# Kernel optimization log

Measured on AMD Instinct MI355X. Metric: run time of the kernel, lower is better.

The kernel has to match this reference:

```python
import jax, jax.numpy as jnp
import numpy as np

NUM_HEADS = 16
HEAD_DIM = 64
LN_EPS = 1e-5


def setup_inputs() -> dict:
    key = jax.random.key(0)
    k1, k2, k3, k4 = jax.random.split(key, 4)
    B, N, D = 4, 2048, NUM_HEADS * HEAD_DIM
    q = jax.random.normal(k1, (B, N, D), dtype=jnp.float32)
    k = jax.random.normal(k2, (B, N, D), dtype=jnp.float32)
    v = jax.random.normal(k3, (B, N, D), dtype=jnp.float32)
    W_out = jax.random.normal(k4, (D, D), dtype=jnp.float32) * (1.0 / np.sqrt(D))
    g = jnp.ones((D,), dtype=jnp.float32)
    return {"q": q, "k": k, "v": v, "W_out": W_out, "g": g}


def _split_heads(x):
    b, n, _ = x.shape
    return x.reshape(b, n, NUM_HEADS, HEAD_DIM).transpose(0, 2, 1, 3)  # b h n d


def reference(q, k, v, W_out, g):
    scale = HEAD_DIM ** -0.5
    qh = _split_heads(q) * scale          # [b,h,n,d]
    kh = _split_heads(k)                  # [b,h,m,d]
    vh = _split_heads(v)                  # [b,h,m,d]
    sim = jnp.einsum('bhnd,bhmd->bhnm', qh, kh)
    attn = jax.nn.softmax(sim.astype(jnp.float32), axis=-1)
    out = jnp.einsum('bhnm,bhmd->bhnd', attn, vh)
    b, h, n, d = out.shape
    out = out.transpose(0, 2, 1, 3).reshape(b, n, h * d)  # b n (h d)
    out = out @ W_out.T                   # Linear, no bias
    # LayerNorm (bias=False), biased variance
    mean = jnp.mean(out, axis=-1, keepdims=True)
    var = jnp.var(out, axis=-1, keepdims=True)
    return (out - mean) * jax.lax.rsqrt(var + LN_EPS) * g
```

## Files before the change

kernel.cpp:

```cpp
#include <hip/hip_runtime.h>
#include <hip/hip_bf16.h>


#define Bv 4
#define Nv 2048
#define Hv 16
#define DHv 64
#define Dv 1024
#define NT (Nv / 64)

typedef __attribute__((ext_vector_type(8))) short short8;
typedef __attribute__((ext_vector_type(4))) float floatx4;

__device__ inline unsigned pack_bf2(float a, float b) {
    unsigned ua = __builtin_bit_cast(unsigned, a) + 0x8000u;
    unsigned ub = __builtin_bit_cast(unsigned, b) + 0x8000u;
    return __builtin_amdgcn_perm(ub, ua, 0x07060302u);
}

__global__ __launch_bounds__(256)
void attn_mfma(const float* __restrict__ q,
               const float* __restrict__ k,
               const float* __restrict__ v,
               __hip_bfloat16* __restrict__ out) {
    __shared__ __align__(16) short Kt[2][64 * 64];
    __shared__ __align__(16) short Vt[2][64 * 64];

    const int t = threadIdx.x;
    const int wave = t >> 6, lane = t & 63;
    const int quad = lane >> 4, lr = lane & 15;
    const int b = blockIdx.z, h = blockIdx.y;
    const int q0 = blockIdx.x * 128;
    const size_t bh = ((size_t)b * Nv) * Dv + h * DHv;

    float4 kpre[2][2], vpre[2][2];
    auto load_tile = [&](int k0) {
#pragma unroll
        for (int p = 0; p < 2; ++p) {
            int idx = p * 256 + t;
            int r = idx >> 3, cb = idx & 7;
            const float* kp = k + bh + (size_t)(k0 + r) * Dv + cb * 8;
            kpre[p][0] = *(const float4*)kp;
            kpre[p][1] = *(const float4*)(kp + 4);
            int dq = idx & 15, rr = idx >> 4;
            const float* vp = v + bh + (size_t)(k0 + 2 * rr) * Dv + dq * 4;
            vpre[p][0] = *(const float4*)vp;
            vpre[p][1] = *(const float4*)(vp + Dv);
        }
    };
    auto store_tile = [&](int buf) {
#pragma unroll
        for (int p = 0; p < 2; ++p) {
            int idx = p * 256 + t;
            int r = idx >> 3, cb = idx & 7;
            uint4 u;
            u.x = pack_bf2(kpre[p][0].x, kpre[p][0].y);
            u.y = pack_bf2(kpre[p][0].z, kpre[p][0].w);
            u.z = pack_bf2(kpre[p][1].x, kpre[p][1].y);
            u.w = pack_bf2(kpre[p][1].z, kpre[p][1].w);
            *(uint4*)&Kt[buf][r * 64 + ((cb ^ (r & 7)) << 3)] = u;
            int dq = idx & 15, rr = idx >> 4;
            float va[4] = {vpre[p][0].x, vpre[p][0].y, vpre[p][0].z, vpre[p][0].w};
            float vb[4] = {vpre[p][1].x, vpre[p][1].y, vpre[p][1].z, vpre[p][1].w};
#pragma unroll
            for (int i = 0; i < 4; ++i) {
                int d = dq * 4 + i;
                ((unsigned*)Vt[buf])[d * 32 + (((rr >> 2) ^ ((d >> 1) & 7)) << 2) + (rr & 3)] =
                    pack_bf2(va[i], vb[i]);
            }
        }
    };

    load_tile(0);

    short8 qfrag[2][2];
#pragma unroll
    for (int qs = 0; qs < 2; ++qs)
#pragma unroll
        for (int kh = 0; kh < 2; ++kh) {
            int row = q0 + wave * 32 + qs * 16 + lr;
            const float* qp = q + bh + (size_t)row * Dv + kh * 32 + quad * 8;
            float4 f0 = *(const float4*)qp;
            float4 f1 = *(const float4*)(qp + 4);
            int4 qi;
            qi.x = (int)pack_bf2(f0.x * 0.125f, f0.y * 0.125f);
            qi.y = (int)pack_bf2(f0.z * 0.125f, f0.w * 0.125f);
            qi.z = (int)pack_bf2(f1.x * 0.125f, f1.y * 0.125f);
            qi.w = (int)pack_bf2(f1.z * 0.125f, f1.w * 0.125f);
            qfrag[qs][kh] = __builtin_bit_cast(short8, qi);
        }

    store_tile(0);

    floatx4 o_acc[2][4] = {};
    float mrow[2] = {-INFINITY, -INFINITY};
    float lrow[2] = {0.f, 0.f};
    const int srcA = ((2 * (quad & 1)) << 4) | lr;
    const int srcB = srcA + 16;
    const bool hi = (quad >= 2);

    for (int it = 0; it < NT; ++it) {
        const int cur = it & 1;
        __syncthreads();
        if (it + 1 < NT) load_tile((it + 1) * 64);

        floatx4 s_acc[2][4] = {};
#pragma unroll
        for (int tt = 0; tt < 4; ++tt) {
            int row = tt * 16 + lr;
            short8 kf0 = *(const short8*)&Kt[cur][row * 64 + ((quad ^ (lr & 7)) << 3)];
            short8 kf1 = *(const short8*)&Kt[cur][row * 64 + (((4 + quad) ^ (lr & 7)) << 3)];
#pragma unroll
            for (int qs = 0; qs < 2; ++qs) {
                s_acc[qs][tt] = __builtin_amdgcn_mfma_f32_16x16x32_bf16(kf0, qfrag[qs][0], s_acc[qs][tt], 0, 0, 0);
                s_acc[qs][tt] = __builtin_amdgcn_mfma_f32_16x16x32_bf16(kf1, qfrag[qs][1], s_acc[qs][tt], 0, 0, 0);
            }
        }

        unsigned p2[2][8];
#pragma unroll
        for (int qs = 0; qs < 2; ++qs) {
            float tmax = -INFINITY;
#pragma unroll
            for (int tt = 0; tt < 4; ++tt)
#pragma unroll
                for (int r2 = 0; r2 < 4; ++r2) tmax = fmaxf(tmax, s_acc[qs][tt][r2]);
            tmax = fmaxf(tmax, __shfl_xor(tmax, 16));
            tmax = fmaxf(tmax, __shfl_xor(tmax, 32));
            float mnew = fmaxf(mrow[qs], tmax);
            float alpha = __expf(mrow[qs] - mnew);
            mrow[qs] = mnew;
            float psum = 0.f;
#pragma unroll
            for (int tt = 0; tt < 4; ++tt)
#pragma unroll
                for (int r2 = 0; r2 < 4; ++r2) {
                    float p = __expf(s_acc[qs][tt][r2] - mnew);
                    s_acc[qs][tt][r2] = p;
                    psum += p;
                }
            psum += __shfl_xor(psum, 16);
            psum += __shfl_xor(psum, 32);
            lrow[qs] = lrow[qs] * alpha + psum;
#pragma unroll
            for (int r2 = 0; r2 < 4; ++r2) {
                float ar = __shfl(alpha, quad * 4 + r2);
#pragma unroll
                for (int td = 0; td < 4; ++td) o_acc[qs][td][r2] *= ar;
            }
#pragma unroll
            for (int tt = 0; tt < 4; ++tt) {
                p2[qs][tt * 2 + 0] = pack_bf2(s_acc[qs][tt][0], s_acc[qs][tt][1]);
                p2[qs][tt * 2 + 1] = pack_bf2(s_acc[qs][tt][2], s_acc[qs][tt][3]);
            }
        }

#pragma unroll
        for (int kh = 0; kh < 2; ++kh) {
            short8 af[2];
#pragma unroll
            for (int qs = 0; qs < 2; ++qs) {
                int tlo = 4 * kh, thi = 4 * kh + 2;
                unsigned d0a = __shfl(p2[qs][tlo + 0], srcA), d0b = __shfl(p2[qs][thi + 0], srcA);
                unsigned d1a = __shfl(p2[qs][tlo + 1], srcA), d1b = __shfl(p2[qs][thi + 1], srcA);
                unsigned d2a = __shfl(p2[qs][tlo + 0], srcB), d2b = __shfl(p2[qs][thi + 0], srcB);
                unsigned d3a = __shfl(p2[qs][tlo + 1], srcB), d3b = __shfl(p2[qs][thi + 1], srcB);
                int4 afi;
                afi.x = (int)(hi ? d0b : d0a);
                afi.y = (int)(hi ? d1b : d1a);
                afi.z = (int)(hi ? d2b : d2a);
                afi.w = (int)(hi ? d3b : d3a);
                af[qs] = __builtin_bit_cast(short8, afi);
            }
#pragma unroll
            for (int td = 0; td < 4; ++td) {
                int d = td * 16 + lr;
                short8 vf = *(const short8*)&Vt[cur][d * 64 + (((kh * 4 + quad) ^ (lr >> 1)) << 3)];
                o_acc[0][td] = __builtin_amdgcn_mfma_f32_16x16x32_bf16(af[0], vf, o_acc[0][td], 0, 0, 0);
                o_acc[1][td] = __builtin_amdgcn_mfma_f32_16x16x32_bf16(af[1], vf, o_acc[1][td], 0, 0, 0);
            }
        }

        if (it + 1 < NT) store_tile(1 - cur);
    }

#pragma unroll
    for (int qs = 0; qs < 2; ++qs) {
        float linv = 1.f / lrow[qs];
#pragma unroll
        for (int r2 = 0; r2 < 4; ++r2) {
            float lv = __shfl(linv, quad * 4 + r2);
            int row = q0 + wave * 32 + qs * 16 + quad * 4 + r2;
            size_t base = ((size_t)(b * Nv + row)) * Dv + h * DHv;
#pragma unroll
            for (int td = 0; td < 4; ++td)
                out[base + td * 16 + lr] = __float2bfloat16(o_acc[qs][td][r2] * lv);
        }
    }
}

__global__ __launch_bounds__(256)
void proj_kernel(const __hip_bfloat16* __restrict__ A,
                 const float* __restrict__ W,
                 float* __restrict__ C) {
    __shared__ __align__(16) short As[2][128 * 32];
    __shared__ __align__(16) short Ws[2][128 * 32];

    const int t = threadIdx.x;
    const int wave = t >> 6, lane = t & 63;
    const int quad = lane >> 4, lr = lane & 15;
    const int wm = wave >> 1, wn = wave & 1;
    const int bm = blockIdx.y * 128;
    const int bn = blockIdx.x * 128;

    floatx4 acc[4][4] = {};

    const int rA = t >> 2;
    const int cbA = t & 3;

    uint4 apre[2];
    float4 wpre[2][2];
    auto load_t = [&](int k0) {
#pragma unroll
        for (int p = 0; p < 2; ++p) {
            int r = rA + p * 64;
            apre[p] = *(const uint4*)(A + (size_t)(bm + r) * Dv + k0 + cbA * 8);
            const float* wp = W + (size_t)(bn + r) * Dv + k0 + cbA * 8;
            wpre[p][0] = *(const float4*)wp;
            wpre[p][1] = *(const float4*)(wp + 4);
        }
    };
    auto store_t = [&](int buf) {
#pragma unroll
        for (int p = 0; p < 2; ++p) {
            int r = rA + p * 64;
            *(uint4*)&As[buf][r * 32 + cbA * 8] = apre[p];
            uint4 u;
            u.x = pack_bf2(wpre[p][0].x, wpre[p][0].y);
            u.y = pack_bf2(wpre[p][0].z, wpre[p][0].w);
            u.z = pack_bf2(wpre[p][1].x, wpre[p][1].y);
            u.w = pack_bf2(wpre[p][1].z, wpre[p][1].w);
            *(uint4*)&Ws[buf][r * 32 + cbA * 8] = u;
        }
    };

    load_t(0);
    store_t(0);

    for (int it = 0; it < Dv / 32; ++it) {
        const int cur = it & 1;
        __syncthreads();
        if (it + 1 < Dv / 32) load_t((it + 1) * 32);

        short8 af[4];
#pragma unroll
        for (int mb = 0; mb < 4; ++mb)
            af[mb] = *(const short8*)&As[cur][(wm * 64 + mb * 16 + lr) * 32 + quad * 8];
#pragma unroll
        for (int nb = 0; nb < 4; ++nb) {
            short8 bf = *(const short8*)&Ws[cur][(wn * 64 + nb * 16 + lr) * 32 + quad * 8];
#pragma unroll
            for (int mb = 0; mb < 4; ++mb)
                acc[mb][nb] = __builtin_amdgcn_mfma_f32_16x16x32_bf16(af[mb], bf, acc[mb][nb], 0, 0, 0);
        }

        if (it + 1 < Dv / 32) store_t(1 - cur);
    }

#pragma unroll
    for (int mb = 0; mb < 4; ++mb)
#pragma unroll
        for (int nb = 0; nb < 4; ++nb) {
            int row = bm + wm * 64 + mb * 16 + quad * 4;
            int col = bn + wn * 64 + nb * 16 + lr;
#pragma unroll
            for (int r = 0; r < 4; ++r)
                C[(size_t)(row + r) * Dv + col] = acc[mb][nb][r];
        }
}

__global__ __launch_bounds__(256)
void ln_kernel(float* __restrict__ C,
               const float* __restrict__ g) {
    const int row = blockIdx.x;
    const int t = threadIdx.x;
    const int wave = t >> 6, lane = t & 63;

    float* rp = C + (size_t)row * Dv;
    float4 x = *(const float4*)(rp + t * 4);

    float s = x.x + x.y + x.z + x.w;
    float sq = x.x * x.x + x.y * x.y + x.z * x.z + x.w * x.w;
#pragma unroll
    for (int off = 32; off >= 1; off >>= 1) {
        s += __shfl_xor(s, off);
        sq += __shfl_xor(sq, off);
    }
    __shared__ float ss[4], ssq[4];
    if (lane == 0) { ss[wave] = s; ssq[wave] = sq; }
    __syncthreads();
    s = ss[0] + ss[1] + ss[2] + ss[3];
    sq = ssq[0] + ssq[1] + ssq[2] + ssq[3];

    const float rn = 1.f / (float)Dv;
    float mean = s * rn;
    float var = sq * rn - mean * mean;
    float inv = rsqrtf(var + 1e-5f);

    float4 gv = *(const float4*)(g + t * 4);

    float4 o;
    o.x = (x.x - mean) * inv * gv.x;
    o.y = (x.y - mean) * inv * gv.y;
    o.z = (x.z - mean) * inv * gv.z;
    o.w = (x.w - mean) * inv * gv.w;
    *(float4*)(rp + t * 4) = o;
}

extern "C" void kernel_launch(void* const* d_in, const int* in_sizes, int n_in,
                              void* d_out, int out_size, void* d_ws, size_t ws_size,
                              hipStream_t stream) {
    const float* q = (const float*)d_in[0];
    const float* k = (const float*)d_in[1];
    const float* v = (const float*)d_in[2];
    const float* W = (const float*)d_in[3];
    const float* g = (const float*)d_in[4];
    float* out = (float*)d_out;

    __hip_bfloat16* attn = (__hip_bfloat16*)d_ws;

    attn_mfma<<<dim3(Nv / 128, Hv, Bv), 256, 0, stream>>>(q, k, v, attn);
    proj_kernel<<<dim3(Dv / 128, (Bv * Nv) / 128), 256, 0, stream>>>(attn, W, out);
    ln_kernel<<<Bv * Nv, 256, 0, stream>>>(out, g);
}
```

Before: 337.5 us.

## Pre-convert W to bf16 and stream projection tiles via direct global-to-LDS loads

Adds a small kernel that converts W_out to bf16 once per call into workspace. A new projection GEMM uses global_load_lds to move A and W tiles straight into XOR-swizzled LDS with a K-tile of 64 and double buffering. This removes the per-tile fp32-to-bf16 conversion and register staging in the GEMM, and halves W traffic. The cost is an extra kernel launch and workspace use. The old fp32-W path is kept as a fallback when the workspace is too small.

```diff
diff --git a/kernel.cpp b/kernel.cpp
--- a/kernel.cpp
+++ b/kernel.cpp
@@ -200,9 +200,95 @@
 }
 
 __global__ __launch_bounds__(256)
+void wconv_kernel(const float* __restrict__ W, __hip_bfloat16* __restrict__ Wb) {
+    int base = (blockIdx.x * 256 + threadIdx.x) * 8;
+    float4 f0 = *(const float4*)(W + base);
+    float4 f1 = *(const float4*)(W + base + 4);
+    uint4 u;
+    u.x = pack_bf2(f0.x, f0.y);
+    u.y = pack_bf2(f0.z, f0.w);
+    u.z = pack_bf2(f1.x, f1.y);
+    u.w = pack_bf2(f1.z, f1.w);
+    *(uint4*)(Wb + base) = u;
+}
+
+__global__ __launch_bounds__(256)
 void proj_kernel(const __hip_bfloat16* __restrict__ A,
-                 const float* __restrict__ W,
+                 const __hip_bfloat16* __restrict__ Wb,
                  float* __restrict__ C) {
+    __shared__ __align__(16) short As[2][128 * 64];
+    __shared__ __align__(16) short Ws[2][128 * 64];
+
+    const int t = threadIdx.x;
+    const int wave = t >> 6, lane = t & 63;
+    const int quad = lane >> 4, lr = lane & 15;
+    const int wm = wave >> 1, wn = wave & 1;
+    const int bm = blockIdx.y * 128;
+    const int bn = blockIdx.x * 128;
+
+    floatx4 acc[4][4] = {};
+
+    auto stage = [&](int buf, int k0) {
+#pragma unroll
+        for (int c = 0; c < 4; ++c) {
+            const int blk = c * 4 + wave;
+            const int r = blk * 8 + (lane >> 3);
+            const int g = (lane & 7) ^ (r & 7);
+            const __hip_bfloat16* ga = A + (size_t)(bm + r) * Dv + k0 + g * 8;
+            const __hip_bfloat16* gw = Wb + (size_t)(bn + r) * Dv + k0 + g * 8;
+            __builtin_amdgcn_global_load_lds(
+                (const __attribute__((address_space(1))) unsigned int*)(const void*)ga,
+                (__attribute__((address_space(3))) unsigned int*)(void*)&As[buf][blk * 512],
+                16, 0, 0);
+            __builtin_amdgcn_global_load_lds(
+                (const __attribute__((address_space(1))) unsigned int*)(const void*)gw,
+                (__attribute__((address_space(3))) unsigned int*)(void*)&Ws[buf][blk * 512],
+                16, 0, 0);
+        }
+    };
+
+    stage(0, 0);
+
+    for (int it = 0; it < Dv / 64; ++it) {
+        const int cur = it & 1;
+        __syncthreads();
+        if (it + 1 < Dv / 64) stage(1 - cur, (it + 1) * 64);
+
+#pragma unroll
+        for (int ks = 0; ks < 2; ++ks) {
+            short8 af[4];
+#pragma unroll
+            for (int mb = 0; mb < 4; ++mb) {
+                int row = wm * 64 + mb * 16 + lr;
+                af[mb] = *(const short8*)&As[cur][row * 64 + (((ks * 4 + quad) ^ (lr & 7)) << 3)];
+            }
+#pragma unroll
+            for (int nb = 0; nb < 4; ++nb) {
+                int row = wn * 64 + nb * 16 + lr;
+                short8 bf = *(const short8*)&Ws[cur][row * 64 + (((ks * 4 + quad) ^ (lr & 7)) << 3)];
+#pragma unroll
+                for (int mb = 0; mb < 4; ++mb)
+                    acc[mb][nb] = __builtin_amdgcn_mfma_f32_16x16x32_bf16(af[mb], bf, acc[mb][nb], 0, 0, 0);
+            }
+        }
+    }
+
+#pragma unroll
+    for (int mb = 0; mb < 4; ++mb)
+#pragma unroll
+        for (int nb = 0; nb < 4; ++nb) {
+            int row = bm + wm * 64 + mb * 16 + quad * 4;
+            int col = bn + wn * 64 + nb * 16 + lr;
+#pragma unroll
+            for (int r = 0; r < 4; ++r)
+                C[(size_t)(row + r) * Dv + col] = acc[mb][nb][r];
+        }
+}
+
+__global__ __launch_bounds__(256)
+void proj_kernel_f32w(const __hip_bfloat16* __restrict__ A,
+                      const float* __restrict__ W,
+                      float* __restrict__ C) {
     __shared__ __align__(16) short As[2][128 * 32];
     __shared__ __align__(16) short Ws[2][128 * 32];
 
@@ -327,9 +413,20 @@
     const float* g = (const float*)d_in[4];
     float* out = (float*)d_out;
 
+    const size_t attnBytes = (size_t)Bv * Nv * Dv * 2;
+    const size_t wbBytes = (size_t)Dv * Dv * 2;
+
     __hip_bfloat16* attn = (__hip_bfloat16*)d_ws;
 
     attn_mfma<<<dim3(Nv / 128, Hv, Bv), 256, 0, stream>>>(q, k, v, attn);
-    proj_kernel<<<dim3(Dv / 128, (Bv * Nv) / 128), 256, 0, stream>>>(attn, W, out);
+
+    if (ws_size >= attnBytes + wbBytes) {
+        __hip_bfloat16* Wb = (__hip_bfloat16*)((char*)d_ws + attnBytes);
+        wconv_kernel<<<512, 256, 0, stream>>>(W, Wb);
+        proj_kernel<<<dim3(Dv / 128, (Bv * Nv) / 128), 256, 0, stream>>>(attn, Wb, out);
+    } else {
+        proj_kernel_f32w<<<dim3(Dv / 128, (Bv * Nv) / 128), 256, 0, stream>>>(attn, W, out);
+    }
+
     ln_kernel<<<Bv * Nv, 256, 0, stream>>>(out, g);
 }
```

Result: faster. 318.8 us (-5.5%).

## Pre-convert K, V, W to bf16 and stage tiles via direct global-to-LDS loads

Applied to the files above, without the earlier changes.

Adds a prep kernel that converts K and W to bf16 and writes V transposed per head in bf16. The attention and projection kernels then fill LDS with global_load_lds DMA into swizzled layouts, with no register round-trip or per-tile conversion. The projection K-step grows to 64, attention blocks are remapped so heads group by XCD, and shuffle-based reductions and P-fragment exchanges use permlane swaps. This costs an extra kernel launch and an extra read and write of K, V and W through workspace memory.

```diff
diff --git a/kernel.cpp b/kernel.cpp
--- a/kernel.cpp
+++ b/kernel.cpp
@@ -9,6 +9,10 @@
 #define Dv 1024
 #define NT (Nv / 64)
 
+#define KCONV_BLOCKS 4096
+#define WCONV_BLOCKS 512
+#define VT_BLOCKS 2048
+
 typedef __attribute__((ext_vector_type(8))) short short8;
 typedef __attribute__((ext_vector_type(4))) float floatx4;
 
@@ -18,60 +22,125 @@
     return __builtin_amdgcn_perm(ub, ua, 0x07060302u);
 }
 
+__device__ inline void plswap16(unsigned &a, unsigned &b) {
+    auto r = __builtin_amdgcn_permlane16_swap(a, b, false, false);
+    a = r[0]; b = r[1];
+}
+__device__ inline void plswap32(unsigned &a, unsigned &b) {
+    auto r = __builtin_amdgcn_permlane32_swap(a, b, false, false);
+    a = r[0]; b = r[1];
+}
+
+__device__ inline float redq_max(float x) {
+    unsigned a = __builtin_bit_cast(unsigned, x), b = a;
+    plswap16(a, b);
+    float m = fmaxf(__builtin_bit_cast(float, a), __builtin_bit_cast(float, b));
+    unsigned c = __builtin_bit_cast(unsigned, m), d = c;
+    plswap32(c, d);
+    return fmaxf(__builtin_bit_cast(float, c), __builtin_bit_cast(float, d));
+}
+__device__ inline float redq_sum(float x) {
+    unsigned a = __builtin_bit_cast(unsigned, x), b = a;
+    plswap16(a, b);
+    float m = __builtin_bit_cast(float, a) + __builtin_bit_cast(float, b);
+    unsigned c = __builtin_bit_cast(unsigned, m), d = c;
+    plswap32(c, d);
+    return __builtin_bit_cast(float, c) + __builtin_bit_cast(float, d);
+}
+
 __global__ __launch_bounds__(256)
-void attn_mfma(const float* __restrict__ q,
-               const float* __restrict__ k,
-               const float* __restrict__ v,
-               __hip_bfloat16* __restrict__ out) {
+void prep_all(const float* __restrict__ K, __hip_bfloat16* __restrict__ Kb,
+              const float* __restrict__ W, __hip_bfloat16* __restrict__ Wb,
+              const float* __restrict__ v, __hip_bfloat16* __restrict__ vt) {
+    __shared__ short T[64][72];
+    int bid = blockIdx.x;
+    if (bid < KCONV_BLOCKS + WCONV_BLOCKS) {
+        const float* src;
+        __hip_bfloat16* dst;
+        if (bid < KCONV_BLOCKS) { src = K; dst = Kb; }
+        else { src = W; dst = Wb; bid -= KCONV_BLOCKS; }
+        int base = (bid * 256 + threadIdx.x) * 8;
+        float4 f0 = *(const float4*)(src + base);
+        float4 f1 = *(const float4*)(src + base + 4);
+        uint4 u;
+        u.x = pack_bf2(f0.x, f0.y);
+        u.y = pack_bf2(f0.z, f0.w);
+        u.z = pack_bf2(f1.x, f1.y);
+        u.w = pack_bf2(f1.z, f1.w);
+        *(uint4*)(dst + base) = u;
+        return;
+    }
+    bid -= KCONV_BLOCKS + WCONV_BLOCKS;
+    const int b = bid >> 9;
+    const int rem = bid & 511;
+    const int h = rem >> 5;
+    const int n0 = (rem & 31) * 64;
+    const int t = threadIdx.x;
+    const int ir = t >> 4;
+    const int d4 = (t & 15) * 4;
+#pragma unroll
+    for (int pass = 0; pass < 4; ++pass) {
+        int n = pass * 16 + ir;
+        float4 f = *(const float4*)(v + ((size_t)b * Nv + n0 + n) * Dv + h * DHv + d4);
+        T[d4 + 0][n] = (short)(pack_bf2(f.x, f.x) & 0xffffu);
+        T[d4 + 1][n] = (short)(pack_bf2(f.y, f.y) & 0xffffu);
+        T[d4 + 2][n] = (short)(pack_bf2(f.z, f.z) & 0xffffu);
+        T[d4 + 3][n] = (short)(pack_bf2(f.w, f.w) & 0xffffu);
+    }
+    __syncthreads();
+    const int d = t >> 2, kg = (t & 3) * 16;
+    unsigned u[8];
+#pragma unroll
+    for (int i = 0; i < 8; ++i)
+        u[i] = (unsigned)(unsigned short)T[d][kg + 2 * i] |
+               ((unsigned)(unsigned short)T[d][kg + 2 * i + 1] << 16);
+    __hip_bfloat16* op = vt + ((size_t)(b * Hv + h) * DHv + d) * Nv + n0 + kg;
+    *(uint4*)op = *(uint4*)&u[0];
+    *(uint4*)(op + 8) = *(uint4*)&u[4];
+}
+
+__global__ __launch_bounds__(256)
+void attn_mfma_pre(const float* __restrict__ q,
+                   const __hip_bfloat16* __restrict__ Kb,
+                   const __hip_bfloat16* __restrict__ Vtb,
+                   __hip_bfloat16* __restrict__ out) {
     __shared__ __align__(16) short Kt[2][64 * 64];
     __shared__ __align__(16) short Vt[2][64 * 64];
 
     const int t = threadIdx.x;
     const int wave = t >> 6, lane = t & 63;
     const int quad = lane >> 4, lr = lane & 15;
-    const int b = blockIdx.z, h = blockIdx.y;
-    const int q0 = blockIdx.x * 128;
-    const size_t bh = ((size_t)b * Nv) * Dv + h * DHv;
-
-    float4 kpre[2][2], vpre[2][2];
-    auto load_tile = [&](int k0) {
-#pragma unroll
-        for (int p = 0; p < 2; ++p) {
-            int idx = p * 256 + t;
-            int r = idx >> 3, cb = idx & 7;
-            const float* kp = k + bh + (size_t)(k0 + r) * Dv + cb * 8;
-            kpre[p][0] = *(const float4*)kp;
-            kpre[p][1] = *(const float4*)(kp + 4);
-            int dq = idx & 15, rr = idx >> 4;
-            const float* vp = v + bh + (size_t)(k0 + 2 * rr) * Dv + dq * 4;
-            vpre[p][0] = *(const float4*)vp;
-            vpre[p][1] = *(const float4*)(vp + Dv);
+    const int b = blockIdx.z;
+    const int lid2 = blockIdx.y * 16 + blockIdx.x;
+    const int xcd = lid2 & 7, jj = lid2 >> 3;
+    const int h = xcd * 2 + (jj >> 4);
+    const int q0 = (jj & 15) * 128;
+    const size_t qbh = ((size_t)b * Nv) * Dv + h * DHv;
+    const __hip_bfloat16* kb = Kb + (size_t)b * Nv * Dv + h * DHv;
+    const __hip_bfloat16* vtb = Vtb + (size_t)(b * Hv + h) * DHv * Nv;
+
+    const int srow = lane >> 3;
+    const int sg = lane & 7;
+    auto stage = [&](int buf, int k0) {
+#pragma unroll
+        for (int c = 0; c < 2; ++c) {
+            int blk = wave * 2 + c;
+            int r = blk * 8 + srow;
+            int g = sg ^ (r & 7);
+            __builtin_amdgcn_global_load_lds(
+                (const __attribute__((address_space(1))) unsigned*)(const void*)
+                    (kb + (size_t)(k0 + r) * Dv + g * 8),
+                (__attribute__((address_space(3))) unsigned*)(void*)&Kt[buf][blk * 512],
+                16, 0, 0);
+            __builtin_amdgcn_global_load_lds(
+                (const __attribute__((address_space(1))) unsigned*)(const void*)
+                    (vtb + (size_t)r * Nv + k0 + g * 8),
+                (__attribute__((address_space(3))) unsigned*)(void*)&Vt[buf][blk * 512],
+                16, 0, 0);
         }
     };
-    auto store_tile = [&](int buf) {
-#pragma unroll
-        for (int p = 0; p < 2; ++p) {
-            int idx = p * 256 + t;
-            int r = idx >> 3, cb = idx & 7;
-            uint4 u;
-            u.x = pack_bf2(kpre[p][0].x, kpre[p][0].y);
-            u.y = pack_bf2(kpre[p][0].z, kpre[p][0].w);
-            u.z = pack_bf2(kpre[p][1].x, kpre[p][1].y);
-            u.w = pack_bf2(kpre[p][1].z, kpre[p][1].w);
-            *(uint4*)&Kt[buf][r * 64 + ((cb ^ (r & 7)) << 3)] = u;
-            int dq = idx & 15, rr = idx >> 4;
-            float va[4] = {vpre[p][0].x, vpre[p][0].y, vpre[p][0].z, vpre[p][0].w};
-            float vb[4] = {vpre[p][1].x, vpre[p][1].y, vpre[p][1].z, vpre[p][1].w};
-#pragma unroll
-            for (int i = 0; i < 4; ++i) {
-                int d = dq * 4 + i;
-                ((unsigned*)Vt[buf])[d * 32 + (((rr >> 2) ^ ((d >> 1) & 7)) << 2) + (rr & 3)] =
-                    pack_bf2(va[i], vb[i]);
-            }
-        }
-    };
-
-    load_tile(0);
+
+    stage(0, 0);
 
     short8 qfrag[2][2];
 #pragma unroll
@@ -79,7 +148,7 @@
 #pragma unroll
         for (int kh = 0; kh < 2; ++kh) {
             int row = q0 + wave * 32 + qs * 16 + lr;
-            const float* qp = q + bh + (size_t)row * Dv + kh * 32 + quad * 8;
+            const float* qp = q + qbh + (size_t)row * Dv + kh * 32 + quad * 8;
             float4 f0 = *(const float4*)qp;
             float4 f1 = *(const float4*)(qp + 4);
             int4 qi;
@@ -90,19 +159,14 @@
             qfrag[qs][kh] = __builtin_bit_cast(short8, qi);
         }
 
-    store_tile(0);
-
     floatx4 o_acc[2][4] = {};
     float mrow[2] = {-INFINITY, -INFINITY};
     float lrow[2] = {0.f, 0.f};
-    const int srcA = ((2 * (quad & 1)) << 4) | lr;
-    const int srcB = srcA + 16;
-    const bool hi = (quad >= 2);
 
     for (int it = 0; it < NT; ++it) {
         const int cur = it & 1;
         __syncthreads();
-        if (it + 1 < NT) load_tile((it + 1) * 64);
+        if (it + 1 < NT) stage(1 - cur, (it + 1) * 64);
 
         floatx4 s_acc[2][4] = {};
 #pragma unroll
@@ -120,13 +184,13 @@
         unsigned p2[2][8];
 #pragma unroll
         for (int qs = 0; qs < 2; ++qs) {
-            float tmax = -INFINITY;
+            float t4[4];
 #pragma unroll
             for (int tt = 0; tt < 4; ++tt)
-#pragma unroll
-                for (int r2 = 0; r2 < 4; ++r2) tmax = fmaxf(tmax, s_acc[qs][tt][r2]);
-            tmax = fmaxf(tmax, __shfl_xor(tmax, 16));
-            tmax = fmaxf(tmax, __shfl_xor(tmax, 32));
+                t4[tt] = fmaxf(fmaxf(s_acc[qs][tt][0], s_acc[qs][tt][1]),
+                               fmaxf(s_acc[qs][tt][2], s_acc[qs][tt][3]));
+            float tmax = fmaxf(fmaxf(t4[0], t4[1]), fmaxf(t4[2], t4[3]));
+            tmax = redq_max(tmax);
             float mnew = fmaxf(mrow[qs], tmax);
             float alpha = __expf(mrow[qs] - mnew);
             mrow[qs] = mnew;
@@ -139,8 +203,7 @@
                     s_acc[qs][tt][r2] = p;
                     psum += p;
                 }
-            psum += __shfl_xor(psum, 16);
-            psum += __shfl_xor(psum, 32);
+            psum = redq_sum(psum);
             lrow[qs] = lrow[qs] * alpha + psum;
 #pragma unroll
             for (int r2 = 0; r2 < 4; ++r2) {
@@ -161,27 +224,27 @@
 #pragma unroll
             for (int qs = 0; qs < 2; ++qs) {
                 int tlo = 4 * kh, thi = 4 * kh + 2;
-                unsigned d0a = __shfl(p2[qs][tlo + 0], srcA), d0b = __shfl(p2[qs][thi + 0], srcA);
-                unsigned d1a = __shfl(p2[qs][tlo + 1], srcA), d1b = __shfl(p2[qs][thi + 1], srcA);
-                unsigned d2a = __shfl(p2[qs][tlo + 0], srcB), d2b = __shfl(p2[qs][thi + 0], srcB);
-                unsigned d3a = __shfl(p2[qs][tlo + 1], srcB), d3b = __shfl(p2[qs][thi + 1], srcB);
+                unsigned a0 = p2[qs][tlo + 0], b0 = p2[qs][thi + 0];
+                unsigned a1 = p2[qs][tlo + 1], b1 = p2[qs][thi + 1];
+                plswap32(a0, b0);
+                plswap16(a0, b0);
+                plswap32(a1, b1);
+                plswap16(a1, b1);
                 int4 afi;
-                afi.x = (int)(hi ? d0b : d0a);
-                afi.y = (int)(hi ? d1b : d1a);
-                afi.z = (int)(hi ? d2b : d2a);
-                afi.w = (int)(hi ? d3b : d3a);
+                afi.x = (int)a0;
+                afi.y = (int)a1;
+                afi.z = (int)b0;
+                afi.w = (int)b1;
                 af[qs] = __builtin_bit_cast(short8, afi);
             }
 #pragma unroll
             for (int td = 0; td < 4; ++td) {
                 int d = td * 16 + lr;
-                short8 vf = *(const short8*)&Vt[cur][d * 64 + (((kh * 4 + quad) ^ (lr >> 1)) << 3)];
+                short8 vf = *(const short8*)&Vt[cur][d * 64 + (((kh * 4 + quad) ^ (lr & 7)) << 3)];
                 o_acc[0][td] = __builtin_amdgcn_mfma_f32_16x16x32_bf16(af[0], vf, o_acc[0][td], 0, 0, 0);
                 o_acc[1][td] = __builtin_amdgcn_mfma_f32_16x16x32_bf16(af[1], vf, o_acc[1][td], 0, 0, 0);
             }
         }
-
-        if (it + 1 < NT) store_tile(1 - cur);
     }
 
 #pragma unroll
@@ -201,10 +264,10 @@
 
 __global__ __launch_bounds__(256)
 void proj_kernel(const __hip_bfloat16* __restrict__ A,
-                 const float* __restrict__ W,
+                 const __hip_bfloat16* __restrict__ Wb,
                  float* __restrict__ C) {
-    __shared__ __align__(16) short As[2][128 * 32];
-    __shared__ __align__(16) short Ws[2][128 * 32];
+    __shared__ __align__(16) short As[2][128 * 64];
+    __shared__ __align__(16) short Ws[2][128 * 64];
 
     const int t = threadIdx.x;
     const int wave = t >> 6, lane = t & 63;
@@ -215,56 +278,49 @@
 
     floatx4 acc[4][4] = {};
 
-    const int rA = t >> 2;
-    const int cbA = t & 3;
-
-    uint4 apre[2];
-    float4 wpre[2][2];
-    auto load_t = [&](int k0) {
-#pragma unroll
-        for (int p = 0; p < 2; ++p) {
-            int r = rA + p * 64;
-            apre[p] = *(const uint4*)(A + (size_t)(bm + r) * Dv + k0 + cbA * 8);
-            const float* wp = W + (size_t)(bn + r) * Dv + k0 + cbA * 8;
-            wpre[p][0] = *(const float4*)wp;
-            wpre[p][1] = *(const float4*)(wp + 4);
+    auto stage = [&](int buf, int k0) {
+#pragma unroll
+        for (int c = 0; c < 4; ++c) {
+            const int blk = c * 4 + wave;
+            const int r = blk * 8 + (lane >> 3);
+            const int g = (lane & 7) ^ (r & 7);
+            const __hip_bfloat16* ga = A + (size_t)(bm + r) * Dv + k0 + g * 8;
+            const __hip_bfloat16* gw = Wb + (size_t)(bn + r) * Dv + k0 + g * 8;
+            __builtin_amdgcn_global_load_lds(
+                (const __attribute__((address_space(1))) unsigned int*)(const void*)ga,
+                (__attribute__((address_space(3))) unsigned int*)(void*)&As[buf][blk * 512],
+                16, 0, 0);
+            __builtin_amdgcn_global_load_lds(
+                (const __attribute__((address_space(1))) unsigned int*)(const void*)gw,
+                (__attribute__((address_space(3))) unsigned int*)(void*)&Ws[buf][blk * 512],
+                16, 0, 0);
         }
     };
-    auto store_t = [&](int buf) {
-#pragma unroll
-        for (int p = 0; p < 2; ++p) {
-            int r = rA + p * 64;
-            *(uint4*)&As[buf][r * 32 + cbA * 8] = apre[p];
-            uint4 u;
-            u.x = pack_bf2(wpre[p][0].x, wpre[p][0].y);
-            u.y = pack_bf2(wpre[p][0].z, wpre[p][0].w);
-            u.z = pack_bf2(wpre[p][1].x, wpre[p][1].y);
-            u.w = pack_bf2(wpre[p][1].z, wpre[p][1].w);
-            *(uint4*)&Ws[buf][r * 32 + cbA * 8] = u;
-        }
-    };
-
-    load_t(0);
-    store_t(0);
-
-    for (int it = 0; it < Dv / 32; ++it) {
+
+    stage(0, 0);
+
+    for (int it = 0; it < Dv / 64; ++it) {
         const int cur = it & 1;
         __syncthreads();
-        if (it + 1 < Dv / 32) load_t((it + 1) * 32);
-
-        short8 af[4];
-#pragma unroll
-        for (int mb = 0; mb < 4; ++mb)
-            af[mb] = *(const short8*)&As[cur][(wm * 64 + mb * 16 + lr) * 32 + quad * 8];
-#pragma unroll
-        for (int nb = 0; nb < 4; ++nb) {
-            short8 bf = *(const short8*)&Ws[cur][(wn * 64 + nb * 16 + lr) * 32 + quad * 8];
-#pragma unroll
-            for (int mb = 0; mb < 4; ++mb)
-                acc[mb][nb] = __builtin_amdgcn_mfma_f32_16x16x32_bf16(af[mb], bf, acc[mb][nb], 0, 0, 0);
-        }
-
-        if (it + 1 < Dv / 32) store_t(1 - cur);
+        if (it + 1 < Dv / 64) stage(1 - cur, (it + 1) * 64);
+
+#pragma unroll
+        for (int ks = 0; ks < 2; ++ks) {
+            short8 af[4];
+#pragma unroll
+            for (int mb = 0; mb < 4; ++mb) {
+                int row = wm * 64 + mb * 16 + lr;
+                af[mb] = *(const short8*)&As[cur][row * 64 + (((ks * 4 + quad) ^ (lr & 7)) << 3)];
+            }
+#pragma unroll
+            for (int nb = 0; nb < 4; ++nb) {
+                int row = wn * 64 + nb * 16 + lr;
+                short8 bf = *(const short8*)&Ws[cur][row * 64 + (((ks * 4 + quad) ^ (lr & 7)) << 3)];
+#pragma unroll
+                for (int mb = 0; mb < 4; ++mb)
+                    acc[mb][nb] = __builtin_amdgcn_mfma_f32_16x16x32_bf16(af[mb], bf, acc[mb][nb], 0, 0, 0);
+            }
+        }
     }
 
 #pragma unroll
@@ -327,9 +383,17 @@
     const float* g = (const float*)d_in[4];
     float* out = (float*)d_out;
 
+    const size_t attnB = (size_t)Bv * Nv * Dv * 2;
+    const size_t wbB = (size_t)Dv * Dv * 2;
+    const size_t kbB = (size_t)Bv * Nv * Dv * 2;
+
     __hip_bfloat16* attn = (__hip_bfloat16*)d_ws;
-
-    attn_mfma<<<dim3(Nv / 128, Hv, Bv), 256, 0, stream>>>(q, k, v, attn);
-    proj_kernel<<<dim3(Dv / 128, (Bv * Nv) / 128), 256, 0, stream>>>(attn, W, out);
+    __hip_bfloat16* Wb = (__hip_bfloat16*)((char*)d_ws + attnB);
+    __hip_bfloat16* Kb = (__hip_bfloat16*)((char*)d_ws + attnB + wbB);
+    __hip_bfloat16* Vtb = (__hip_bfloat16*)((char*)d_ws + attnB + wbB + kbB);
+
+    prep_all<<<KCONV_BLOCKS + WCONV_BLOCKS + VT_BLOCKS, 256, 0, stream>>>(k, Kb, W, Wb, v, Vtb);
+    attn_mfma_pre<<<dim3(16, 16, Bv), 256, 0, stream>>>(q, Kb, Vtb, attn);
+    proj_kernel<<<dim3(Dv / 128, (Bv * Nv) / 128), 256, 0, stream>>>(attn, Wb, out);
     ln_kernel<<<Bv * Nv, 256, 0, stream>>>(out, g);
 }
```

Result: faster. 317.7 us (-5.8%).
